# Kernel optimization log

Measured on AMD Instinct MI355X. Metric: run time of the kernel, lower is better.

## Reference

```python
import jax, jax.numpy as jnp
import numpy as np

N_ATOMS = 131072
N_EDGES = 524288
N_MOLS = 2048
D = 128      # n_atom_basis
F = 128      # n_filters
G = 50       # n_gaussians
T = 3        # interaction blocks
CUTOFF = 5.0
LOG2 = float(np.log(2.0))


def ssp(x):
    # shifted softplus: ln(0.5*e^x + 0.5) = softplus(x) - ln 2
    return jax.nn.softplus(x) - LOG2


def setup_inputs() -> dict:
    key = jax.random.key(0)
    ks = jax.random.split(key, 20)
    s = 0.05
    z = jax.random.randint(ks[0], (N_ATOMS,), 1, 100, dtype=jnp.int32)
    xyz = jax.random.normal(ks[1], (N_ATOMS, 3), dtype=jnp.float32) * 3.0
    a0 = jax.random.randint(ks[2], (N_EDGES,), 0, N_ATOMS, dtype=jnp.int32)
    off = jax.random.randint(ks[3], (N_EDGES,), 1, N_ATOMS, dtype=jnp.int32)
    a = jnp.stack([a0, (a0 + off) % N_ATOMS], axis=1)  # distinct endpoints
    mol_id = jnp.sort(jax.random.randint(ks[4], (N_ATOMS,), 0, N_MOLS, dtype=jnp.int32))
    emb = (jax.random.normal(ks[5], (100, D)) * s).at[0].set(0.0)  # padding_idx=0
    return dict(
        xyz=xyz,
        emb=emb,
        fw1=jax.random.normal(ks[6], (T, G, F)) * s,
        fb1=jnp.zeros((T, F)),
        fw2=jax.random.normal(ks[7], (T, F, F)) * s,
        fb2=jnp.zeros((T, F)),
        win=jax.random.normal(ks[8], (T, D, F)) * s,
        wout1=jax.random.normal(ks[9], (T, F, D)) * s,
        bout1=jnp.zeros((T, D)),
        wout2=jax.random.normal(ks[10], (T, D, D)) * s,
        bout2=jnp.zeros((T, D)),
        wa1=jax.random.normal(ks[11], (D, D // 2)) * s,
        ba1=jnp.zeros((D // 2,)),
        wa2=jax.random.normal(ks[12], (D // 2, 1)) * s,
        ba2=jnp.zeros((1,)),
        z=z, a=a, mol_id=mol_id,
    )


def reference(xyz, emb, fw1, fb1, fw2, fb2, win, wout1, bout1, wout2, bout2,
              wa1, ba1, wa2, ba2, z, a, mol_id):
    r = emb[z]                                            # [N, D] atom embeddings
    # edge distances: e = ||xyz[a0] - xyz[a1]||  -> [E, 1]
    d = jnp.sqrt(((xyz[a[:, 0]] - xyz[a[:, 1]]) ** 2).sum(-1))[:, None]
    # Gaussian smearing on [0, cutoff]
    offsets = jnp.linspace(0.0, CUTOFF, G)
    width = offsets[1] - offsets[0]
    g = jnp.exp((-0.5 / width ** 2) * (d - offsets) ** 2)  # [E, G]
    # smooth cosine cutoff (cutoff_soft)
    C = 0.5 * (jnp.cos(d * jnp.pi / CUTOFF) + 1.0)          # [E, 1]
    for t in range(T):
        # continuous filter network on edge features
        W = ssp(g @ fw1[t] + fb1[t]) @ fw2[t] + fb2[t]      # [E, F]
        W = W * C
        h = r @ win[t]                                      # in2f, no bias [N, F]
        # symmetric gather-filter-scatter over undirected edge list
        y = jnp.zeros_like(h)
        y = y.at[a[:, 0]].add(h[a[:, 1]] * W)
        y = y.at[a[:, 1]].add(h[a[:, 0]] * W)
        dr = ssp(y @ wout1[t] + bout1[t]) @ wout2[t] + bout2[t]
        r = r + dr                                          # residual update
    # atomwise energy head
    r = ssp(r @ wa1 + ba1) @ wa2 + ba2                      # [N, 1]
    # per-molecule sum pooling (torch.split + sum)
    return jax.ops.segment_sum(r, mol_id, num_segments=N_MOLS)  # [N_MOLS, 1]
```

## Files before the change

kernel.cpp:

```cpp
#include <hip/hip_runtime.h>
#include <hip/hip_bf16.h>

#define N_ATOMS 131072
#define N_EDGES 524288
#define N_MOLS  2048
#define DD      128
#define FF      128
#define GG      50
#define TT      3

typedef __hip_bfloat16 bf16;
typedef __attribute__((ext_vector_type(8))) short short8;
typedef __attribute__((ext_vector_type(4))) float floatx4;

__device__ __forceinline__ float b2f(bf16 v) { return __bfloat162float(v); }
__device__ __forceinline__ bf16  f2b(float v) { return __float2bfloat16(v); }

__device__ __forceinline__ unsigned short f2bu(float f) {
    unsigned u = __float_as_uint(f);
    u += 0x7fff + ((u >> 16) & 1);
    return (unsigned short)(u >> 16);
}
__device__ __forceinline__ bf16 f2b_fast(float f) {
    union { unsigned short u; bf16 b; } c; c.u = f2bu(f); return c.b;
}
__device__ __forceinline__ unsigned int pk2(float lo, float hi) {
    return ((unsigned)f2bu(hi) << 16) | f2bu(lo);
}

__device__ __forceinline__ float2 up2(unsigned int u) {
    float2 f;
    f.x = __uint_as_float(u << 16);
    f.y = __uint_as_float(u & 0xffff0000u);
    return f;
}

__device__ __forceinline__ float sspf(float x) {
    float e = __expf(-fabsf(x));
    return fmaxf(x, 0.f) + __logf(1.f + e) - 0.69314718056f;
}

__device__ __forceinline__ void fma8(float* ac, uint4 wv, uint4 hv) {
    float2 w0 = up2(wv.x), h0 = up2(hv.x);
    float2 w1 = up2(wv.y), h1 = up2(hv.y);
    float2 w2 = up2(wv.z), h2 = up2(hv.z);
    float2 w3 = up2(wv.w), h3 = up2(hv.w);
    ac[0] = fmaf(w0.x, h0.x, ac[0]); ac[1] = fmaf(w0.y, h0.y, ac[1]);
    ac[2] = fmaf(w1.x, h1.x, ac[2]); ac[3] = fmaf(w1.y, h1.y, ac[3]);
    ac[4] = fmaf(w2.x, h2.x, ac[4]); ac[5] = fmaf(w2.y, h2.y, ac[5]);
    ac[6] = fmaf(w3.x, h3.x, ac[6]); ac[7] = fmaf(w3.y, h3.y, ac[7]);
}

template <int NCT>
__device__ __forceinline__ void mfma_half(const bf16* A, const bf16* B,
                                          floatx4 (&acc)[2][NCT],
                                          int kA, int wave, int q, int ln) {
#pragma unroll
    for (int k0 = 0; k0 < 64; k0 += 32) {
        short8 a0 = *(const short8*)(A + (wave * 32 + ln) * 136 + kA + k0 + q * 8);
        short8 a1 = *(const short8*)(A + (wave * 32 + 16 + ln) * 136 + kA + k0 + q * 8);
#pragma unroll
        for (int ct = 0; ct < NCT; ct++) {
            short8 b = *(const short8*)(B + (ct * 16 + ln) * 72 + k0 + q * 8);
            acc[0][ct] = __builtin_amdgcn_mfma_f32_16x16x32_bf16(a0, b, acc[0][ct], 0, 0, 0);
            acc[1][ct] = __builtin_amdgcn_mfma_f32_16x16x32_bf16(a1, b, acc[1][ct], 0, 0, 0);
        }
    }
}

template <int NCT>
__device__ __forceinline__ void mfma_halfo(const bf16* A, const bf16* B,
                                           floatx4 (&acc)[2][8], int ctBase,
                                           int kA, int wave, int q, int ln) {
#pragma unroll
    for (int k0 = 0; k0 < 64; k0 += 32) {
        short8 a0 = *(const short8*)(A + (wave * 32 + ln) * 136 + kA + k0 + q * 8);
        short8 a1 = *(const short8*)(A + (wave * 32 + 16 + ln) * 136 + kA + k0 + q * 8);
#pragma unroll
        for (int ct = 0; ct < NCT; ct++) {
            short8 b = *(const short8*)(B + (ct * 16 + ln) * 72 + k0 + q * 8);
            acc[0][ctBase + ct] = __builtin_amdgcn_mfma_f32_16x16x32_bf16(a0, b, acc[0][ctBase + ct], 0, 0, 0);
            acc[1][ctBase + ct] = __builtin_amdgcn_mfma_f32_16x16x32_bf16(a1, b, acc[1][ctBase + ct], 0, 0, 0);
        }
    }
}

template <int NCT>
__device__ __forceinline__ void mfma64(const bf16* A, const bf16* B,
                                       floatx4 (&acc)[NCT],
                                       int kA, int wave, int q, int ln) {
#pragma unroll
    for (int k0 = 0; k0 < 64; k0 += 32) {
        short8 a = *(const short8*)(A + (wave * 16 + ln) * 136 + kA + k0 + q * 8);
#pragma unroll
        for (int ct = 0; ct < NCT; ct++) {
            short8 b = *(const short8*)(B + (ct * 16 + ln) * 72 + k0 + q * 8);
            acc[ct] = __builtin_amdgcn_mfma_f32_16x16x32_bf16(a, b, acc[ct], 0, 0, 0);
        }
    }
}

__device__ __forceinline__ void stage_b(bf16* B, const bf16* WT, int k0,
                                        int nrows, int ldk, int tid) {
    for (int i = tid; i < nrows * 8; i += 256) {
        int n = i >> 3, kc = i & 7;
        *(short8*)(B + n * 72 + kc * 8) =
            *(const short8*)(WT + n * ldk + k0 + kc * 8);
    }
}

__global__ __launch_bounds__(256) void k_initwt(const float* __restrict__ emb,
                                                const int* __restrict__ z,
                                                bf16* __restrict__ rb,
                                                const float* __restrict__ fw1,
                                                const float* __restrict__ fw2,
                                                const float* __restrict__ win,
                                                const float* __restrict__ wout1,
                                                const float* __restrict__ wout2,
                                                const float* __restrict__ wa1,
                                                bf16* __restrict__ fw1T, bf16* __restrict__ fw2T,
                                                bf16* __restrict__ winT, bf16* __restrict__ wout1T,
                                                bf16* __restrict__ wout2T, bf16* __restrict__ wa1T) {
    int bi = blockIdx.x;
    if (bi < N_ATOMS * 16 / 256) {
        int idx = bi * 256 + threadIdx.x;
        int atom = idx >> 4, seg = idx & 15;
        const float* src = emb + (size_t)z[atom] * DD + seg * 8;
        float4 v0 = *(const float4*)(src);
        float4 v1 = *(const float4*)(src + 4);
        uint4 o;
        o.x = pk2(v0.x, v0.y); o.y = pk2(v0.z, v0.w);
        o.z = pk2(v1.x, v1.y); o.w = pk2(v1.z, v1.w);
        *(uint4*)(rb + (size_t)atom * DD + seg * 8) = o;
        return;
    }
    int idx = (bi - N_ATOMS * 16 / 256) * 256 + threadIdx.x;
    if (idx < 3 * 128 * 64) {
        int t = idx / 8192, j = idx % 8192;
        int n = j >> 6, k = j & 63;
        fw1T[idx] = (k < GG) ? f2b(fw1[t * GG * FF + k * FF + n]) : f2b(0.f);
        return;
    }
    idx -= 3 * 128 * 64;
    if (idx < 3 * 16384) { int t = idx / 16384, j = idx % 16384; int n = j >> 7, k = j & 127;
        fw2T[idx] = f2b(fw2[t * 16384 + k * 128 + n]); return; }
    idx -= 3 * 16384;
    if (idx < 3 * 16384) { int t = idx / 16384, j = idx % 16384; int n = j >> 7, k = j & 127;
        winT[idx] = f2b(win[t * 16384 + k * 128 + n]); return; }
    idx -= 3 * 16384;
    if (idx < 3 * 16384) { int t = idx / 16384, j = idx % 16384; int n = j >> 7, k = j & 127;
        wout1T[idx] = f2b(wout1[t * 16384 + k * 128 + n]); return; }
    idx -= 3 * 16384;
    if (idx < 3 * 16384) { int t = idx / 16384, j = idx % 16384; int n = j >> 7, k = j & 127;
        wout2T[idx] = f2b(wout2[t * 16384 + k * 128 + n]); return; }
    idx -= 3 * 16384;
    if (idx < 64 * 128) { int n = idx >> 7, k = idx & 127;
        wa1T[idx] = f2b(wa1[k * 64 + n]); return; }
}

__global__ __launch_bounds__(256) void k_dist(const float* __restrict__ xyz,
                                              const int* __restrict__ a,
                                              float* __restrict__ dArr,
                                              float* __restrict__ cArr,
                                              float* __restrict__ molE) {
    int e = blockIdx.x * 256 + threadIdx.x;
    if (e < N_MOLS) molE[e] = 0.f;
    int A0 = a[2 * e], A1 = a[2 * e + 1];
    float dx = xyz[3 * A0]     - xyz[3 * A1];
    float dy = xyz[3 * A0 + 1] - xyz[3 * A1 + 1];
    float dz = xyz[3 * A0 + 2] - xyz[3 * A1 + 2];
    float d = sqrtf(dx * dx + dy * dy + dz * dz);
    dArr[e] = d;
    cArr[e] = 0.5f * (__cosf(d * 0.6283185307179586f) + 1.f);
}

__global__ __launch_bounds__(256) void k_zero2(int* __restrict__ pA,
                                               int* __restrict__ p1) {
    int i = blockIdx.x * 256 + threadIdx.x;
    if (i < N_ATOMS) pA[i] = 0;
    else p1[i - N_ATOMS] = 0;
}

__global__ __launch_bounds__(256) void k_count2(const int* __restrict__ a,
                                                int* __restrict__ cntA,
                                                int* __restrict__ cnt1,
                                                float* __restrict__ molE) {
    int e = blockIdx.x * 256 + threadIdx.x;
    if (e < N_MOLS) molE[e] = 0.f;
    atomicAdd(&cntA[a[2 * e]], 1);
    atomicAdd(&cnt1[a[2 * e + 1]], 1);
}

__global__ __launch_bounds__(256) void k_scan1j(const int* __restrict__ cursorA,
                                                const int* __restrict__ cursor1,
                                                int* __restrict__ bsumA,
                                                int* __restrict__ bsum1) {
    __shared__ int red[256];
    int tid = threadIdx.x;
    int arr = blockIdx.x >> 8, b = blockIdx.x & 255;
    const int* counts = arr ? cursor1 : cursorA;
    int* bsum = arr ? bsum1 : bsumA;
    int i0 = b * 512 + tid * 2;
    red[tid] = counts[i0] + counts[i0 + 1];
    __syncthreads();
    for (int off = 128; off > 0; off >>= 1) {
        if (tid < off) red[tid] += red[tid + off];
        __syncthreads();
    }
    if (tid == 0) bsum[b] = red[0];
}

__global__ __launch_bounds__(256) void k_scan2j(int* __restrict__ bsumA,
                                                int* __restrict__ bsum1,
                                                int* __restrict__ baseA,
                                                int* __restrict__ ptr1) {
    __shared__ int v[256];
    int tid = threadIdx.x;
    for (int arr = 0; arr < 2; arr++) {
        int* bsum = arr ? bsum1 : bsumA;
        int* ptrN = arr ? ptr1 : baseA;
        v[tid] = bsum[tid];
        __syncthreads();
        if (tid == 0) {
            int acc = 0;
            for (int i = 0; i < 256; i++) { int t = v[i]; v[i] = acc; acc += t; }
            ptrN[N_ATOMS] = acc;
        }
        __syncthreads();
        bsum[tid] = v[tid];
        __syncthreads();
    }
}

__global__ __launch_bounds__(256) void k_scan3j(int* __restrict__ cursorA,
                                                int* __restrict__ cursor1,
                                                const int* __restrict__ bsumA,
                                                const int* __restrict__ bsum1,
                                                int* __restrict__ baseA,
                                                int* __restrict__ ptr1) {
    __shared__ int red[256];
    int tid = threadIdx.x;
    int arr = blockIdx.x >> 8, b = blockIdx.x & 255;
    int* counts = arr ? cursor1 : cursorA;
    const int* bsum = arr ? bsum1 : bsumA;
    int* ptr = arr ? ptr1 : baseA;
    int i0 = b * 512 + tid * 2;
    int c0 = counts[i0], c1 = counts[i0 + 1];
    int s = c0 + c1;
    red[tid] = s;
    __syncthreads();
    for (int off = 1; off < 256; off <<= 1) {
        int t = (tid >= off) ? red[tid - off] : 0;
        __syncthreads();
        red[tid] += t;
        __syncthreads();
    }
    int base = bsum[b] + red[tid] - s;
    ptr[i0] = base;
    ptr[i0 + 1] = base + c0;
    counts[i0] = base;
    counts[i0 + 1] = base + c0;
}

__global__ __launch_bounds__(256) void k_permA(const float* __restrict__ xyz,
                                               const int* __restrict__ a,
                                               int* __restrict__ cursorA,
                                               int* __restrict__ cursor1,
                                               float* __restrict__ dAp,
                                               float* __restrict__ cAp,
                                               int* __restrict__ a1s,
                                               int* __restrict__ adj1) {
    int e = blockIdx.x * 256 + threadIdx.x;
    int A0 = a[2 * e], A1 = a[2 * e + 1];
    float dx = xyz[3 * A0]     - xyz[3 * A1];
    float dy = xyz[3 * A0 + 1] - xyz[3 * A1 + 1];
    float dz = xyz[3 * A0 + 2] - xyz[3 * A1 + 2];
    float d = sqrtf(dx * dx + dy * dy + dz * dz);
    int newe = atomicAdd(&cursorA[A0], 1);
    dAp[newe] = d;
    cAp[newe] = 0.5f * (__cosf(d * 0.6283185307179586f) + 1.f);
    a1s[newe] = A1;
    int slot = atomicAdd(&cursor1[A1], 1);
    adj1[2 * slot] = newe;
    adj1[2 * slot + 1] = A0;
}

struct SmemHE {
    bf16 A[128][136];
    bf16 B[64][72];
    float dS[128], cS[128], b1S[128], b2S[128];
};

__device__ __forceinline__ void h_part128(SmemHE& sm, int blk,
                                          const bf16* __restrict__ rb,
                                          const bf16* __restrict__ winT_t,
                                          bf16* __restrict__ h) {
    int tid = threadIdx.x, n0 = blk * 128;
    for (int i = tid; i < 128 * 16; i += 256) {
        int row = i >> 4, seg = i & 15;
        *(uint4*)(&sm.A[row][seg * 8]) =
            *(const uint4*)(rb + (size_t)(n0 + row) * DD + seg * 8);
    }
    stage_b(&sm.B[0][0], winT_t, 0, 64, 128, tid);
    __syncthreads();
    int wave = tid >> 6, lane = tid & 63, q = lane >> 4, ln = lane & 15;
    floatx4 acc[2][8];
#pragma unroll
    for (int i = 0; i < 2; i++)
#pragma unroll
        for (int j = 0; j < 8; j++) acc[i][j] = (floatx4){0.f, 0.f, 0.f, 0.f};
    mfma_halfo<4>(&sm.A[0][0], &sm.B[0][0], acc, 0, 0, wave, q, ln);
    __syncthreads();
    stage_b(&sm.B[0][0], winT_t + 64 * 128, 0, 64, 128, tid);
    __syncthreads();
    mfma_halfo<4>(&sm.A[0][0], &sm.B[0][0], acc, 4, 0, wave, q, ln);
    __syncthreads();
    stage_b(&sm.B[0][0], winT_t, 64, 64, 128, tid);
    __syncthreads();
    mfma_halfo<4>(&sm.A[0][0], &sm.B[0][0], acc, 0, 64, wave, q, ln);
    __syncthreads();
    stage_b(&sm.B[0][0], winT_t + 64 * 128, 64, 64, 128, tid);
    __syncthreads();
    mfma_halfo<4>(&sm.A[0][0], &sm.B[0][0], acc, 4, 64, wave, q, ln);
#pragma unroll
    for (int rt = 0; rt < 2; rt++)
#pragma unroll
        for (int cc = 0; cc < 8; cc++)
#pragma unroll
            for (int rg = 0; rg < 4; rg++) {
                int row = wave * 32 + rt * 16 + q * 4 + rg;
                int col = (cc >> 2) * 64 + (cc & 3) * 16 + ln;
                sm.A[row][col] = f2b_fast(acc[rt][cc][rg]);
            }
    __syncthreads();
    for (int i = tid; i < 128 * 16; i += 256) {
        int row = i >> 4, seg = i & 15;
        *(uint4*)(h + (size_t)(n0 + row) * FF + seg * 8) =
            *(const uint4*)(&sm.A[row][seg * 8]);
    }
}

__device__ __forceinline__ void edge_part128(SmemHE& sm, int blk,
                                             const float* __restrict__ dAp,
                                             const float* __restrict__ cAp,
                                             const bf16* __restrict__ fw1T_t,
                                             const float* __restrict__ fb1_t,
                                             const bf16* __restrict__ fw2T_t,
                                             const float* __restrict__ fb2_t,
                                             bf16* __restrict__ Wt) {
    int tid = threadIdx.x, e0 = blk * 128;
    if (tid < 128) {
        sm.dS[tid] = dAp[e0 + tid];
        sm.cS[tid] = cAp[e0 + tid];
        sm.b1S[tid] = fb1_t[tid];
        sm.b2S[tid] = fb2_t[tid];
    }
    stage_b(&sm.B[0][0], fw1T_t, 0, 64, 64, tid);
    __syncthreads();
    const float width = 5.0f / 49.0f;
    const float coeff = -0.5f / (width * width);
    for (int idx = tid; idx < 128 * 32; idx += 256) {
        int i = idx >> 5, kp = (idx & 31) * 2;
        float d = sm.dS[i];
        float t0 = d - (float)kp * width;
        float t1 = d - (float)(kp + 1) * width;
        float v0 = (kp < GG)     ? __expf(coeff * t0 * t0) : 0.f;
        float v1 = (kp + 1 < GG) ? __expf(coeff * t1 * t1) : 0.f;
        *(unsigned int*)(&sm.A[i][kp]) = pk2(v0, v1);
    }
    __syncthreads();
    int wave = tid >> 6, lane = tid & 63, q = lane >> 4, ln = lane & 15;
    floatx4 acc[2][8];
#pragma unroll
    for (int i = 0; i < 2; i++)
#pragma unroll
        for (int j = 0; j < 8; j++) acc[i][j] = (floatx4){0.f, 0.f, 0.f, 0.f};
    mfma_halfo<4>(&sm.A[0][0], &sm.B[0][0], acc, 0, 0, wave, q, ln);
    __syncthreads();
    stage_b(&sm.B[0][0], fw1T_t + 64 * 64, 0, 64, 64, tid);
    __syncthreads();
    mfma_halfo<4>(&sm.A[0][0], &sm.B[0][0], acc, 4, 0, wave, q, ln);
#pragma unroll
    for (int rt = 0; rt < 2; rt++)
#pragma unroll
        for (int cc = 0; cc < 8; cc++)
#pragma unroll
            for (int rg = 0; rg < 4; rg++) {
                int row = wave * 32 + rt * 16 + q * 4 + rg;
                int col = (cc >> 2) * 64 + (cc & 3) * 16 + ln;
                sm.A[row][col] = f2b_fast(sspf(acc[rt][cc][rg] + sm.b1S[col]));
            }
    __syncthreads();
    stage_b(&sm.B[0][0], fw2T_t, 0, 64, 128, tid);
    __syncthreads();
#pragma unroll
    for (int i = 0; i < 2; i++)
#pragma unroll
        for (int j = 0; j < 8; j++) acc[i][j] = (floatx4){0.f, 0.f, 0.f, 0.f};
    mfma_halfo<4>(&sm.A[0][0], &sm.B[0][0], acc, 0, 0, wave, q, ln);
    __syncthreads();
    stage_b(&sm.B[0][0], fw2T_t + 64 * 128, 0, 64, 128, tid);
    __syncthreads();
    mfma_halfo<4>(&sm.A[0][0], &sm.B[0][0], acc, 4, 0, wave, q, ln);
    __syncthreads();
    stage_b(&sm.B[0][0], fw2T_t, 64, 64, 128, tid);
    __syncthreads();
    mfma_halfo<4>(&sm.A[0][0], &sm.B[0][0], acc, 0, 64, wave, q, ln);
    __syncthreads();
    stage_b(&sm.B[0][0], fw2T_t + 64 * 128, 64, 64, 128, tid);
    __syncthreads();
    mfma_halfo<4>(&sm.A[0][0], &sm.B[0][0], acc, 4, 64, wave, q, ln);
#pragma unroll
    for (int rt = 0; rt < 2; rt++)
#pragma unroll
        for (int cc = 0; cc < 8; cc++)
#pragma unroll
            for (int rg = 0; rg < 4; rg++) {
                int row = wave * 32 + rt * 16 + q * 4 + rg;
                int col = (cc >> 2) * 64 + (cc & 3) * 16 + ln;
                sm.A[row][col] = f2b_fast((acc[rt][cc][rg] + sm.b2S[col]) * sm.cS[row]);
            }
    __syncthreads();
    for (int i = tid; i < 128 * 16; i += 256) {
        int row = i >> 4, seg = i & 15;
        *(uint4*)(Wt + (size_t)(e0 + row) * FF + seg * 8) =
            *(const uint4*)(&sm.A[row][seg * 8]);
    }
}

__global__ __launch_bounds__(256, 3) void k_he(const bf16* __restrict__ rb,
                                               const bf16* __restrict__ winT_t,
                                               bf16* __restrict__ h,
                                               const float* __restrict__ dAp,
                                               const float* __restrict__ cAp,
                                               const bf16* __restrict__ fw1T_t,
                                               const float* __restrict__ fb1_t,
                                               const bf16* __restrict__ fw2T_t,
                                               const float* __restrict__ fb2_t,
                                               bf16* __restrict__ Wt) {
    __shared__ SmemHE sm;
    int bi = blockIdx.x;
    if (bi % 5 == 0)
        h_part128(sm, bi / 5, rb, winT_t, h);
    else
        edge_part128(sm, bi - bi / 5 - 1, dAp, cAp, fw1T_t, fb1_t, fw2T_t, fb2_t, Wt);
}

__global__ __launch_bounds__(256, 5) void k_gather_node64(const int* __restrict__ baseA,
                                                          const int* __restrict__ a1s,
                                                          const int* __restrict__ ptr1,
                                                          const int* __restrict__ adj1,
                                                          const bf16* __restrict__ Wt,
                                                          const bf16* __restrict__ h,
                                                          const bf16* __restrict__ wout1T_t,
                                                          const float* __restrict__ bo1_t,
                                                          const bf16* __restrict__ wout2T_t,
                                                          const float* __restrict__ bo2_t,
                                                          bf16* __restrict__ rb) {
    __shared__ __align__(16) bf16 A[64][136];
    __shared__ __align__(16) bf16 B[64][72];
    __shared__ float b1S[128], b2S[128];
    int tid = threadIdx.x, n0 = blockIdx.x * 64;
    if (tid < 128) { b1S[tid] = bo1_t[tid]; b2S[tid] = bo2_t[tid]; }
    stage_b(&B[0][0], wout1T_t, 0, 64, 128, tid);
    int wave = tid >> 6, lane = tid & 63;
    int seg = lane & 15;
    int rg  = lane >> 4;
    for (int k = 0; k < 16; k += 2) {
        int rowA = wave * 16 + k;
        int atomA = n0 + rowA;
        int2 b01 = *(const int2*)(baseA + atomA);
        int b2v = baseA[atomA + 2];
        int2 p01 = *(const int2*)(ptr1 + atomA);
        int p2v = ptr1[atomA + 2];
        int sA0 = b01.x + rg, eA0v = b01.y;
        int sB0 = b01.y + rg, eB0v = b2v;
        int sA1 = p01.x + rg, eA1v = p01.y;
        int sB1 = p01.y + rg, eB1v = p2v;
        int oA = (sA0 < eA0v) ? a1s[sA0] : 0;
        int oB = (sB0 < eB0v) ? a1s[sB0] : 0;
        int2 eoA = (sA1 < eA1v) ? *(const int2*)(adj1 + 2 * sA1) : make_int2(0, 0);
        int2 eoB = (sB1 < eB1v) ? *(const int2*)(adj1 + 2 * sB1) : make_int2(0, 0);
        float acA[8], acB[8];
#pragma unroll
        for (int j = 0; j < 8; j++) { acA[j] = 0.f; acB[j] = 0.f; }
        while ((sA0 < eA0v) | (sA1 < eA1v) | (sB0 < eB0v) | (sB1 < eB1v)) {
            bool pA0 = sA0 < eA0v, pA1 = sA1 < eA1v;
            bool pB0 = sB0 < eB0v, pB1 = sB1 < eB1v;
            uint4 wvA0, hvA0, wvA1, hvA1, wvB0, hvB0, wvB1, hvB1;
            if (pA0) {
                wvA0 = *(const uint4*)(Wt + (size_t)sA0 * FF + seg * 8);
                hvA0 = *(const uint4*)(h + (size_t)oA * FF + seg * 8);
            }
            if (pA1) {
                wvA1 = *(const uint4*)(Wt + (size_t)eoA.x * FF + seg * 8);
                hvA1 = *(const uint4*)(h + (size_t)eoA.y * FF + seg * 8);
            }
            if (pB0) {
                wvB0 = *(const uint4*)(Wt + (size_t)sB0 * FF + seg * 8);
                hvB0 = *(const uint4*)(h + (size_t)oB * FF + seg * 8);
            }
            if (pB1) {
                wvB1 = *(const uint4*)(Wt + (size_t)eoB.x * FF + seg * 8);
                hvB1 = *(const uint4*)(h + (size_t)eoB.y * FF + seg * 8);
            }
            int sA0n = sA0 + 4, sA1n = sA1 + 4, sB0n = sB0 + 4, sB1n = sB1 + 4;
            int oAn = (sA0n < eA0v) ? a1s[sA0n] : 0;
            int oBn = (sB0n < eB0v) ? a1s[sB0n] : 0;
            int2 eoAn = (sA1n < eA1v) ? *(const int2*)(adj1 + 2 * sA1n) : make_int2(0, 0);
            int2 eoBn = (sB1n < eB1v) ? *(const int2*)(adj1 + 2 * sB1n) : make_int2(0, 0);
            if (pA0) fma8(acA, wvA0, hvA0);
            if (pA1) fma8(acA, wvA1, hvA1);
            if (pB0) fma8(acB, wvB0, hvB0);
            if (pB1) fma8(acB, wvB1, hvB1);
            sA0 = sA0n; sA1 = sA1n; sB0 = sB0n; sB1 = sB1n;
            oA = oAn; oB = oBn; eoA = eoAn; eoB = eoBn;
        }
#pragma unroll
        for (int j = 0; j < 8; j++) {
            float vA = acA[j], vB = acB[j];
            vA += __shfl_down(vA, 32); vB += __shfl_down(vB, 32);
            vA += __shfl_down(vA, 16); vB += __shfl_down(vB, 16);
            acA[j] = vA; acB[j] = vB;
        }
        if (rg == 0) {
            uint4 oU;
            oU.x = pk2(acA[0], acA[1]); oU.y = pk2(acA[2], acA[3]);
            oU.z = pk2(acA[4], acA[5]); oU.w = pk2(acA[6], acA[7]);
            *(uint4*)(&A[rowA][seg * 8]) = oU;
            oU.x = pk2(acB[0], acB[1]); oU.y = pk2(acB[2], acB[3]);
            oU.z = pk2(acB[4], acB[5]); oU.w = pk2(acB[6], acB[7]);
            *(uint4*)(&A[rowA + 1][seg * 8]) = oU;
        }
    }
    __syncthreads();
    int q = lane >> 4, ln = lane & 15;
    floatx4 acc[8];
#pragma unroll
    for (int j = 0; j < 8; j++) acc[j] = (floatx4){0.f, 0.f, 0.f, 0.f};
    mfma64<4>(&A[0][0], &B[0][0], *(floatx4(*)[4])(&acc[0]), 0, wave, q, ln);
    __syncthreads();
    stage_b(&B[0][0], wout1T_t + 64 * 128, 0, 64, 128, tid);
    __syncthreads();
    mfma64<4>(&A[0][0], &B[0][0], *(floatx4(*)[4])(&acc[4]), 0, wave, q, ln);
    __syncthreads();
    stage_b(&B[0][0], wout1T_t, 64, 64, 128, tid);
    __syncthreads();
    mfma64<4>(&A[0][0], &B[0][0], *(floatx4(*)[4])(&acc[0]), 64, wave, q, ln);
    __syncthreads();
    stage_b(&B[0][0], wout1T_t + 64 * 128, 64, 64, 128, tid);
    __syncthreads();
    mfma64<4>(&A[0][0], &B[0][0], *(floatx4(*)[4])(&acc[4]), 64, wave, q, ln);
#pragma unroll
    for (int cc = 0; cc < 8; cc++)
#pragma unroll
        for (int rgi = 0; rgi < 4; rgi++) {
            int row = wave * 16 + q * 4 + rgi;
            int col = (cc >> 2) * 64 + (cc & 3) * 16 + ln;
            A[row][col] = f2b_fast(sspf(acc[cc][rgi] + b1S[col]));
        }
    __syncthreads();
    stage_b(&B[0][0], wout2T_t, 0, 64, 128, tid);
    __syncthreads();
#pragma unroll
    for (int j = 0; j < 8; j++) acc[j] = (floatx4){0.f, 0.f, 0.f, 0.f};
    mfma64<4>(&A[0][0], &B[0][0], *(floatx4(*)[4])(&acc[0]), 0, wave, q, ln);
    __syncthreads();
    stage_b(&B[0][0], wout2T_t + 64 * 128, 0, 64, 128, tid);
    __syncthreads();
    mfma64<4>(&A[0][0], &B[0][0], *(floatx4(*)[4])(&acc[4]), 0, wave, q, ln);
    __syncthreads();
    stage_b(&B[0][0], wout2T_t, 64, 64, 128, tid);
    __syncthreads();
    mfma64<4>(&A[0][0], &B[0][0], *(floatx4(*)[4])(&acc[0]), 64, wave, q, ln);
    __syncthreads();
    stage_b(&B[0][0], wout2T_t + 64 * 128, 64, 64, 128, tid);
    __syncthreads();
    mfma64<4>(&A[0][0], &B[0][0], *(floatx4(*)[4])(&acc[4]), 64, wave, q, ln);
#pragma unroll
    for (int cc = 0; cc < 8; cc++)
#pragma unroll
        for (int rgi = 0; rgi < 4; rgi++) {
            int row = wave * 16 + q * 4 + rgi;
            int col = (cc >> 2) * 64 + (cc & 3) * 16 + ln;
            size_t off = (size_t)(n0 + row) * DD + col;
            rb[off] = f2b_fast(b2f(rb[off]) + acc[cc][rgi] + b2S[col]);
        }
}

__global__ __launch_bounds__(256) void k_h(const bf16* __restrict__ rb,
                                           const bf16* __restrict__ winT_t,
                                           bf16* __restrict__ h,
                                           float* __restrict__ y) {
    __shared__ __align__(16) bf16 A[128][136];
    __shared__ __align__(16) bf16 B[128][72];
    int tid = threadIdx.x, n0 = blockIdx.x * 128;
    for (int i = tid; i < 128 * 16; i += 256) {
        int row = i >> 4, seg = i & 15;
        *(uint4*)(&A[row][seg * 8]) =
            *(const uint4*)(rb + (size_t)(n0 + row) * DD + seg * 8);
        *(float4*)(y + (size_t)(n0 + row) * FF + seg * 8) = (float4){0.f, 0.f, 0.f, 0.f};
        *(float4*)(y + (size_t)(n0 + row) * FF + seg * 8 + 4) = (float4){0.f, 0.f, 0.f, 0.f};
    }
    stage_b(&B[0][0], winT_t, 0, 128, 128, tid);
    __syncthreads();
    int wave = tid >> 6, lane = tid & 63, q = lane >> 4, ln = lane & 15;
    floatx4 acc[2][8];
#pragma unroll
    for (int i = 0; i < 2; i++)
#pragma unroll
        for (int j = 0; j < 8; j++) acc[i][j] = (floatx4){0.f, 0.f, 0.f, 0.f};
    mfma_half<8>(&A[0][0], &B[0][0], acc, 0, wave, q, ln);
    __syncthreads();
    stage_b(&B[0][0], winT_t, 64, 128, 128, tid);
    __syncthreads();
    mfma_half<8>(&A[0][0], &B[0][0], acc, 64, wave, q, ln);
#pragma unroll
    for (int rt = 0; rt < 2; rt++)
#pragma unroll
        for (int ct = 0; ct < 8; ct++)
#pragma unroll
            for (int rg = 0; rg < 4; rg++) {
                int row = wave * 32 + rt * 16 + q * 4 + rg, col = ct * 16 + ln;
                h[(size_t)(n0 + row) * FF + col] = f2b(acc[rt][ct][rg]);
            }
}

__global__ __launch_bounds__(256) void k_edge(const float* __restrict__ dArr,
                                              const float* __restrict__ cArr,
                                              const int* __restrict__ a,
                                              const bf16* __restrict__ fw1T_t,
                                              const float* __restrict__ fb1_t,
                                              const bf16* __restrict__ fw2T_t,
                                              const float* __restrict__ fb2_t,
                                              const bf16* __restrict__ h,
                                              float* __restrict__ y) {
    __shared__ __align__(16) bf16 A[128][136];
    __shared__ __align__(16) bf16 B[128][72];
    __shared__ float dS[128], cS[128], b1S[128], b2S[128];
    __shared__ int a0S[128], a1S[128];
    int tid = threadIdx.x, e0 = blockIdx.x * 128;
    if (tid < 128) {
        int e = e0 + tid;
        dS[tid] = dArr[e]; cS[tid] = cArr[e];
        a0S[tid] = a[2 * e]; a1S[tid] = a[2 * e + 1];
        b1S[tid] = fb1_t[tid]; b2S[tid] = fb2_t[tid];
    }
    stage_b(&B[0][0], fw1T_t, 0, 128, 64, tid);
    __syncthreads();
    const float width = 5.0f / 49.0f;
    const float coeff = -0.5f / (width * width);
    for (int idx = tid; idx < 128 * 64; idx += 256) {
        int i = idx >> 6, k = idx & 63;
        float v = 0.f;
        if (k < GG) { float t = dS[i] - (float)k * width; v = __expf(coeff * t * t); }
        A[i][k] = f2b(v);
    }
    __syncthreads();
    int wave = tid >> 6, lane = tid & 63, q = lane >> 4, ln = lane & 15;
    floatx4 acc[2][8];
#pragma unroll
    for (int i = 0; i < 2; i++)
#pragma unroll
        for (int j = 0; j < 8; j++) acc[i][j] = (floatx4){0.f, 0.f, 0.f, 0.f};
    mfma_half<8>(&A[0][0], &B[0][0], acc, 0, wave, q, ln);
#pragma unroll
    for (int rt = 0; rt < 2; rt++)
#pragma unroll
        for (int ct = 0; ct < 8; ct++)
#pragma unroll
            for (int rg = 0; rg < 4; rg++) {
                int row = wave * 32 + rt * 16 + q * 4 + rg, col = ct * 16 + ln;
                A[row][col] = f2b(sspf(acc[rt][ct][rg] + b1S[col]));
            }
    __syncthreads();
    stage_b(&B[0][0], fw2T_t, 0, 128, 128, tid);
    __syncthreads();
#pragma unroll
    for (int i = 0; i < 2; i++)
#pragma unroll
        for (int j = 0; j < 8; j++) acc[i][j] = (floatx4){0.f, 0.f, 0.f, 0.f};
    mfma_half<8>(&A[0][0], &B[0][0], acc, 0, wave, q, ln);
    __syncthreads();
    stage_b(&B[0][0], fw2T_t, 64, 128, 128, tid);
    __syncthreads();
    mfma_half<8>(&A[0][0], &B[0][0], acc, 64, wave, q, ln);
#pragma unroll
    for (int rt = 0; rt < 2; rt++)
#pragma unroll
        for (int ct = 0; ct < 8; ct++)
#pragma unroll
            for (int rg = 0; rg < 4; rg++) {
                int row = wave * 32 + rt * 16 + q * 4 + rg, col = ct * 16 + ln;
                float w = (acc[rt][ct][rg] + b2S[col]) * cS[row];
                int A0 = a0S[row], A1 = a1S[row];
                float h0 = b2f(h[A0 * FF + col]);
                float h1 = b2f(h[A1 * FF + col]);
                atomicAdd(&y[A0 * FF + col], h1 * w);
                atomicAdd(&y[A1 * FF + col], h0 * w);
            }
}

__global__ __launch_bounds__(256) void k_node(const float* __restrict__ y,
                                              const bf16* __restrict__ wout1T_t,
                                              const float* __restrict__ bo1_t,
                                              const bf16* __restrict__ wout2T_t,
                                              const float* __restrict__ bo2_t,
                                              bf16* __restrict__ rb) {
    __shared__ __align__(16) bf16 A[128][136];
    __shared__ __align__(16) bf16 B[128][72];
    __shared__ float b1S[128], b2S[128];
    int tid = threadIdx.x, n0 = blockIdx.x * 128;
    if (tid < 128) { b1S[tid] = bo1_t[tid]; b2S[tid] = bo2_t[tid]; }
    for (int idx = tid; idx < 128 * 128; idx += 256) {
        int row = idx >> 7, col = idx & 127;
        A[row][col] = f2b(y[(size_t)(n0 + row) * FF + col]);
    }
    stage_b(&B[0][0], wout1T_t, 0, 128, 128, tid);
    __syncthreads();
    int wave = tid >> 6, lane = tid & 63, q = lane >> 4, ln = lane & 15;
    floatx4 acc[2][8];
#pragma unroll
    for (int i = 0; i < 2; i++)
#pragma unroll
        for (int j = 0; j < 8; j++) acc[i][j] = (floatx4){0.f, 0.f, 0.f, 0.f};
    mfma_half<8>(&A[0][0], &B[0][0], acc, 0, wave, q, ln);
    __syncthreads();
    stage_b(&B[0][0], wout1T_t, 64, 128, 128, tid);
    __syncthreads();
    mfma_half<8>(&A[0][0], &B[0][0], acc, 64, wave, q, ln);
#pragma unroll
    for (int rt = 0; rt < 2; rt++)
#pragma unroll
        for (int ct = 0; ct < 8; ct++)
#pragma unroll
            for (int rg = 0; rg < 4; rg++) {
                int row = wave * 32 + rt * 16 + q * 4 + rg, col = ct * 16 + ln;
                A[row][col] = f2b(sspf(acc[rt][ct][rg] + b1S[col]));
            }
    __syncthreads();
    stage_b(&B[0][0], wout2T_t, 0, 128, 128, tid);
    __syncthreads();
#pragma unroll
    for (int i = 0; i < 2; i++)
#pragma unroll
        for (int j = 0; j < 8; j++) acc[i][j] = (floatx4){0.f, 0.f, 0.f, 0.f};
    mfma_half<8>(&A[0][0], &B[0][0], acc, 0, wave, q, ln);
    __syncthreads();
    stage_b(&B[0][0], wout2T_t, 64, 128, 128, tid);
    __syncthreads();
    mfma_half<8>(&A[0][0], &B[0][0], acc, 64, wave, q, ln);
#pragma unroll
    for (int rt = 0; rt < 2; rt++)
#pragma unroll
        for (int ct = 0; ct < 8; ct++)
#pragma unroll
            for (int rg = 0; rg < 4; rg++) {
                int row = wave * 32 + rt * 16 + q * 4 + rg, col = ct * 16 + ln;
                size_t off = (size_t)(n0 + row) * DD + col;
                rb[off] = f2b_fast(b2f(rb[off]) + acc[rt][ct][rg] + b2S[col]);
            }
}

__global__ __launch_bounds__(256) void k_head(const bf16* __restrict__ rb,
                                              const bf16* __restrict__ wa1T,
                                              const float* __restrict__ ba1,
                                              const float* __restrict__ wa2,
                                              const float* __restrict__ ba2,
                                              const int* __restrict__ mol,
                                              float* __restrict__ molE) {
    __shared__ __align__(16) bf16 A[128][136];
    __shared__ __align__(16) bf16 B[64][72];
    __shared__ __align__(16) bf16 U[128][72];
    __shared__ float wa2S[64], ba1S[64];
    int tid = threadIdx.x, n0 = blockIdx.x * 128;
    if (tid < 64) { wa2S[tid] = wa2[tid]; ba1S[tid] = ba1[tid]; }
    for (int i = tid; i < 128 * 16; i += 256) {
        int row = i >> 4, seg = i & 15;
        *(uint4*)(&A[row][seg * 8]) =
            *(const uint4*)(rb + (size_t)(n0 + row) * DD + seg * 8);
    }
    stage_b(&B[0][0], wa1T, 0, 64, 128, tid);
    __syncthreads();
    int wave = tid >> 6, lane = tid & 63, q = lane >> 4, ln = lane & 15;
    floatx4 acc[2][4];
#pragma unroll
    for (int i = 0; i < 2; i++)
#pragma unroll
        for (int j = 0; j < 4; j++) acc[i][j] = (floatx4){0.f, 0.f, 0.f, 0.f};
    mfma_half<4>(&A[0][0], &B[0][0], acc, 0, wave, q, ln);
    __syncthreads();
    stage_b(&B[0][0], wa1T, 64, 64, 128, tid);
    __syncthreads();
    mfma_half<4>(&A[0][0], &B[0][0], acc, 64, wave, q, ln);
#pragma unroll
    for (int rt = 0; rt < 2; rt++)
#pragma unroll
        for (int ct = 0; ct < 4; ct++)
#pragma unroll
            for (int rg = 0; rg < 4; rg++) {
                int row = wave * 32 + rt * 16 + q * 4 + rg, col = ct * 16 + ln;
                U[row][col] = f2b_fast(acc[rt][ct][rg] + ba1S[col]);
            }
    __syncthreads();
    if (tid < 128) {
        float s = ba2[0];
#pragma unroll
        for (int j = 0; j < 64; j++) s += sspf(b2f(U[tid][j])) * wa2S[j];
        atomicAdd(&molE[mol[n0 + tid]], s);
    }
}

__global__ __launch_bounds__(256) void k_out(const float* __restrict__ molE,
                                             float* __restrict__ out) {
    int i = blockIdx.x * 256 + threadIdx.x;
    out[i] = molE[i];
}

extern "C" void kernel_launch(void* const* d_in, const int* in_sizes, int n_in,
                              void* d_out, int out_size, void* d_ws, size_t ws_size,
                              hipStream_t stream) {
    const float* xyz   = (const float*)d_in[0];
    const float* emb   = (const float*)d_in[1];
    const float* fw1   = (const float*)d_in[2];
    const float* fb1   = (const float*)d_in[3];
    const float* fw2   = (const float*)d_in[4];
    const float* fb2   = (const float*)d_in[5];
    const float* win   = (const float*)d_in[6];
    const float* wout1 = (const float*)d_in[7];
    const float* bout1 = (const float*)d_in[8];
    const float* wout2 = (const float*)d_in[9];
    const float* bout2 = (const float*)d_in[10];
    const float* wa1   = (const float*)d_in[11];
    const float* ba1   = (const float*)d_in[12];
    const float* wa2   = (const float*)d_in[13];
    const float* ba2   = (const float*)d_in[14];
    const int*  z     = (const int*)d_in[15];
    const int*  a     = (const int*)d_in[16];
    const int*  mol   = (const int*)d_in[17];

    char* ws = (char*)d_ws;
    bf16*  rb   = (bf16*) ws; ws += (size_t)N_ATOMS * DD * 2;
    bf16*  h    = (bf16*) ws; ws += (size_t)N_ATOMS * FF * 2;
    float* molE = (float*)ws; ws += (size_t)N_MOLS * 4;
    float* dAp  = (float*)ws; ws += (size_t)N_EDGES * 4;
    float* cAp  = (float*)ws; ws += (size_t)N_EDGES * 4;
    bf16*  fw1T   = (bf16*)ws; ws += 3 * 128 * 64 * 2;
    bf16*  fw2T   = (bf16*)ws; ws += 3 * 128 * 128 * 2;
    bf16*  winT   = (bf16*)ws; ws += 3 * 128 * 128 * 2;
    bf16*  wout1T = (bf16*)ws; ws += 3 * 128 * 128 * 2;
    bf16*  wout2T = (bf16*)ws; ws += 3 * 128 * 128 * 2;
    bf16*  wa1T   = (bf16*)ws; ws += 64 * 128 * 2;
    char*  csr_base = ws;
    int*   baseA   = (int*)ws; ws += 524320;
    int*   ptr1    = (int*)ws; ws += 524320;
    int*   cursorA = (int*)ws; ws += (size_t)N_ATOMS * 4;
    int*   cursor1 = (int*)ws; ws += (size_t)N_ATOMS * 4;
    int*   a1s     = (int*)ws; ws += (size_t)N_EDGES * 4;
    int*   adj1    = (int*)ws; ws += (size_t)2 * N_EDGES * 4;
    int*   bsumA   = (int*)ws; ws += 1024;
    int*   bsum1   = (int*)ws; ws += 1024;
    bf16*  Wt      = (bf16*)ws; ws += (size_t)N_EDGES * FF * 2;
    size_t need = (size_t)(ws - (char*)d_ws);

    k_initwt<<<N_ATOMS * 16 / 256 + 896, 256, 0, stream>>>(
        emb, z, rb, fw1, fw2, win, wout1, wout2, wa1,
        fw1T, fw2T, winT, wout1T, wout2T, wa1T);

    if (ws_size >= need) {
        k_zero2<<<2 * N_ATOMS / 256, 256, 0, stream>>>(cursorA, cursor1);
        k_count2<<<N_EDGES / 256, 256, 0, stream>>>(a, cursorA, cursor1, molE);
        k_scan1j<<<512, 256, 0, stream>>>(cursorA, cursor1, bsumA, bsum1);
        k_scan2j<<<1, 256, 0, stream>>>(bsumA, bsum1, baseA, ptr1);
        k_scan3j<<<512, 256, 0, stream>>>(cursorA, cursor1, bsumA, bsum1, baseA, ptr1);
        k_permA<<<N_EDGES / 256, 256, 0, stream>>>(xyz, a, cursorA, cursor1,
                                                   dAp, cAp, a1s, adj1);
        for (int t = 0; t < TT; t++) {
            k_he<<<N_ATOMS / 128 + N_EDGES / 128, 256, 0, stream>>>(
                rb, winT + t * 16384, h, dAp, cAp,
                fw1T + t * 8192, fb1 + t * FF,
                fw2T + t * 16384, fb2 + t * FF, Wt);
            k_gather_node64<<<N_ATOMS / 64, 256, 0, stream>>>(
                baseA, a1s, ptr1, adj1, Wt, h,
                wout1T + t * 16384, bout1 + t * DD,
                wout2T + t * 16384, bout2 + t * DD, rb);
        }
    } else {
        float* y = (float*)csr_base;
        k_dist<<<N_EDGES / 256, 256, 0, stream>>>(xyz, a, dAp, cAp, molE);
        for (int t = 0; t < TT; t++) {
            k_h<<<N_ATOMS / 128, 256, 0, stream>>>(rb, winT + t * 16384, h, y);
            k_edge<<<N_EDGES / 128, 256, 0, stream>>>(dAp, cAp, a,
                                                      fw1T + t * 8192, fb1 + t * FF,
                                                      fw2T + t * 16384, fb2 + t * FF, h, y);
            k_node<<<N_ATOMS / 128, 256, 0, stream>>>(y, wout1T + t * 16384, bout1 + t * DD,
                                                      wout2T + t * 16384, bout2 + t * DD, rb);
        }
    }
    k_head<<<N_ATOMS / 128, 256, 0, stream>>>(rb, wa1T, ba1, wa2, ba2, mol, molE);
    k_out<<<N_MOLS / 256, 256, 0, stream>>>(molE, (float*)d_out);
}
```

Measured before the change: 976.5 us.

## Use 512-thread blocks in fused h/edge kernel and drop output copy kernel

The fused h/edge-filter kernel now runs with 512 threads (8 waves), so each wave owns 16 rows of the 128-row tile instead of 32. Its accumulator registers are halved and more waves share the same LDS tile, which is meant to raise occupancy and latency hiding. In exchange, B-fragment reads from LDS are amortized over fewer rows per wave. The aggressive launch-bounds hint may also force register limits or spills. Separately, the molecule energies are accumulated directly into the output buffer, which removes the final copy kernel launch.

```diff
diff --git a/kernel.cpp b/kernel.cpp
--- a/kernel.cpp
+++ b/kernel.cpp
@@ -69,23 +69,6 @@
 }
 
 template <int NCT>
-__device__ __forceinline__ void mfma_halfo(const bf16* A, const bf16* B,
-                                           floatx4 (&acc)[2][8], int ctBase,
-                                           int kA, int wave, int q, int ln) {
-#pragma unroll
-    for (int k0 = 0; k0 < 64; k0 += 32) {
-        short8 a0 = *(const short8*)(A + (wave * 32 + ln) * 136 + kA + k0 + q * 8);
-        short8 a1 = *(const short8*)(A + (wave * 32 + 16 + ln) * 136 + kA + k0 + q * 8);
-#pragma unroll
-        for (int ct = 0; ct < NCT; ct++) {
-            short8 b = *(const short8*)(B + (ct * 16 + ln) * 72 + k0 + q * 8);
-            acc[0][ctBase + ct] = __builtin_amdgcn_mfma_f32_16x16x32_bf16(a0, b, acc[0][ctBase + ct], 0, 0, 0);
-            acc[1][ctBase + ct] = __builtin_amdgcn_mfma_f32_16x16x32_bf16(a1, b, acc[1][ctBase + ct], 0, 0, 0);
-        }
-    }
-}
-
-template <int NCT>
 __device__ __forceinline__ void mfma64(const bf16* A, const bf16* B,
                                        floatx4 (&acc)[NCT],
                                        int kA, int wave, int q, int ln) {
@@ -103,6 +86,15 @@
 __device__ __forceinline__ void stage_b(bf16* B, const bf16* WT, int k0,
                                         int nrows, int ldk, int tid) {
     for (int i = tid; i < nrows * 8; i += 256) {
+        int n = i >> 3, kc = i & 7;
+        *(short8*)(B + n * 72 + kc * 8) =
+            *(const short8*)(WT + n * ldk + k0 + kc * 8);
+    }
+}
+
+__device__ __forceinline__ void stage_b512(bf16* B, const bf16* WT, int k0,
+                                           int nrows, int ldk, int tid) {
+    for (int i = tid; i < nrows * 8; i += 512) {
         int n = i >> 3, kc = i & 7;
         *(short8*)(B + n * 72 + kc * 8) =
             *(const short8*)(WT + n * ldk + k0 + kc * 8);
@@ -291,56 +283,52 @@
     float dS[128], cS[128], b1S[128], b2S[128];
 };
 
-__device__ __forceinline__ void h_part128(SmemHE& sm, int blk,
+__device__ __forceinline__ void h_part512(SmemHE& sm, int blk,
                                           const bf16* __restrict__ rb,
                                           const bf16* __restrict__ winT_t,
                                           bf16* __restrict__ h) {
     int tid = threadIdx.x, n0 = blk * 128;
-    for (int i = tid; i < 128 * 16; i += 256) {
+    for (int i = tid; i < 128 * 16; i += 512) {
         int row = i >> 4, seg = i & 15;
         *(uint4*)(&sm.A[row][seg * 8]) =
             *(const uint4*)(rb + (size_t)(n0 + row) * DD + seg * 8);
     }
-    stage_b(&sm.B[0][0], winT_t, 0, 64, 128, tid);
+    stage_b512(&sm.B[0][0], winT_t, 0, 64, 128, tid);
     __syncthreads();
     int wave = tid >> 6, lane = tid & 63, q = lane >> 4, ln = lane & 15;
-    floatx4 acc[2][8];
-#pragma unroll
-    for (int i = 0; i < 2; i++)
-#pragma unroll
-        for (int j = 0; j < 8; j++) acc[i][j] = (floatx4){0.f, 0.f, 0.f, 0.f};
-    mfma_halfo<4>(&sm.A[0][0], &sm.B[0][0], acc, 0, 0, wave, q, ln);
-    __syncthreads();
-    stage_b(&sm.B[0][0], winT_t + 64 * 128, 0, 64, 128, tid);
-    __syncthreads();
-    mfma_halfo<4>(&sm.A[0][0], &sm.B[0][0], acc, 4, 0, wave, q, ln);
-    __syncthreads();
-    stage_b(&sm.B[0][0], winT_t, 64, 64, 128, tid);
-    __syncthreads();
-    mfma_halfo<4>(&sm.A[0][0], &sm.B[0][0], acc, 0, 64, wave, q, ln);
-    __syncthreads();
-    stage_b(&sm.B[0][0], winT_t + 64 * 128, 64, 64, 128, tid);
-    __syncthreads();
-    mfma_halfo<4>(&sm.A[0][0], &sm.B[0][0], acc, 4, 64, wave, q, ln);
-#pragma unroll
-    for (int rt = 0; rt < 2; rt++)
-#pragma unroll
-        for (int cc = 0; cc < 8; cc++)
-#pragma unroll
-            for (int rg = 0; rg < 4; rg++) {
-                int row = wave * 32 + rt * 16 + q * 4 + rg;
-                int col = (cc >> 2) * 64 + (cc & 3) * 16 + ln;
-                sm.A[row][col] = f2b_fast(acc[rt][cc][rg]);
-            }
-    __syncthreads();
-    for (int i = tid; i < 128 * 16; i += 256) {
+    floatx4 acc[8];
+#pragma unroll
+    for (int j = 0; j < 8; j++) acc[j] = (floatx4){0.f, 0.f, 0.f, 0.f};
+    mfma64<4>(&sm.A[0][0], &sm.B[0][0], *(floatx4(*)[4])(&acc[0]), 0, wave, q, ln);
+    __syncthreads();
+    stage_b512(&sm.B[0][0], winT_t + 64 * 128, 0, 64, 128, tid);
+    __syncthreads();
+    mfma64<4>(&sm.A[0][0], &sm.B[0][0], *(floatx4(*)[4])(&acc[4]), 0, wave, q, ln);
+    __syncthreads();
+    stage_b512(&sm.B[0][0], winT_t, 64, 64, 128, tid);
+    __syncthreads();
+    mfma64<4>(&sm.A[0][0], &sm.B[0][0], *(floatx4(*)[4])(&acc[0]), 64, wave, q, ln);
+    __syncthreads();
+    stage_b512(&sm.B[0][0], winT_t + 64 * 128, 64, 64, 128, tid);
+    __syncthreads();
+    mfma64<4>(&sm.A[0][0], &sm.B[0][0], *(floatx4(*)[4])(&acc[4]), 64, wave, q, ln);
+#pragma unroll
+    for (int cc = 0; cc < 8; cc++)
+#pragma unroll
+        for (int rg = 0; rg < 4; rg++) {
+            int row = wave * 16 + q * 4 + rg;
+            int col = (cc >> 2) * 64 + (cc & 3) * 16 + ln;
+            sm.A[row][col] = f2b_fast(acc[cc][rg]);
+        }
+    __syncthreads();
+    for (int i = tid; i < 128 * 16; i += 512) {
         int row = i >> 4, seg = i & 15;
         *(uint4*)(h + (size_t)(n0 + row) * FF + seg * 8) =
             *(const uint4*)(&sm.A[row][seg * 8]);
     }
 }
 
-__device__ __forceinline__ void edge_part128(SmemHE& sm, int blk,
+__device__ __forceinline__ void edge_part512(SmemHE& sm, int blk,
                                              const float* __restrict__ dAp,
                                              const float* __restrict__ cAp,
                                              const bf16* __restrict__ fw1T_t,
@@ -355,11 +343,11 @@
         sm.b1S[tid] = fb1_t[tid];
         sm.b2S[tid] = fb2_t[tid];
     }
-    stage_b(&sm.B[0][0], fw1T_t, 0, 64, 64, tid);
+    stage_b512(&sm.B[0][0], fw1T_t, 0, 64, 64, tid);
     __syncthreads();
     const float width = 5.0f / 49.0f;
     const float coeff = -0.5f / (width * width);
-    for (int idx = tid; idx < 128 * 32; idx += 256) {
+    for (int idx = tid; idx < 128 * 32; idx += 512) {
         int i = idx >> 5, kp = (idx & 31) * 2;
         float d = sm.dS[i];
         float t0 = d - (float)kp * width;
@@ -370,65 +358,57 @@
     }
     __syncthreads();
     int wave = tid >> 6, lane = tid & 63, q = lane >> 4, ln = lane & 15;
-    floatx4 acc[2][8];
-#pragma unroll
-    for (int i = 0; i < 2; i++)
-#pragma unroll
-        for (int j = 0; j < 8; j++) acc[i][j] = (floatx4){0.f, 0.f, 0.f, 0.f};
-    mfma_halfo<4>(&sm.A[0][0], &sm.B[0][0], acc, 0, 0, wave, q, ln);
-    __syncthreads();
-    stage_b(&sm.B[0][0], fw1T_t + 64 * 64, 0, 64, 64, tid);
-    __syncthreads();
-    mfma_halfo<4>(&sm.A[0][0], &sm.B[0][0], acc, 4, 0, wave, q, ln);
-#pragma unroll
-    for (int rt = 0; rt < 2; rt++)
-#pragma unroll
-        for (int cc = 0; cc < 8; cc++)
-#pragma unroll
-            for (int rg = 0; rg < 4; rg++) {
-                int row = wave * 32 + rt * 16 + q * 4 + rg;
-                int col = (cc >> 2) * 64 + (cc & 3) * 16 + ln;
-                sm.A[row][col] = f2b_fast(sspf(acc[rt][cc][rg] + sm.b1S[col]));
-            }
-    __syncthreads();
-    stage_b(&sm.B[0][0], fw2T_t, 0, 64, 128, tid);
-    __syncthreads();
-#pragma unroll
-    for (int i = 0; i < 2; i++)
-#pragma unroll
-        for (int j = 0; j < 8; j++) acc[i][j] = (floatx4){0.f, 0.f, 0.f, 0.f};
-    mfma_halfo<4>(&sm.A[0][0], &sm.B[0][0], acc, 0, 0, wave, q, ln);
-    __syncthreads();
-    stage_b(&sm.B[0][0], fw2T_t + 64 * 128, 0, 64, 128, tid);
-    __syncthreads();
-    mfma_halfo<4>(&sm.A[0][0], &sm.B[0][0], acc, 4, 0, wave, q, ln);
-    __syncthreads();
-    stage_b(&sm.B[0][0], fw2T_t, 64, 64, 128, tid);
-    __syncthreads();
-    mfma_halfo<4>(&sm.A[0][0], &sm.B[0][0], acc, 0, 64, wave, q, ln);
-    __syncthreads();
-    stage_b(&sm.B[0][0], fw2T_t + 64 * 128, 64, 64, 128, tid);
-    __syncthreads();
-    mfma_halfo<4>(&sm.A[0][0], &sm.B[0][0], acc, 4, 64, wave, q, ln);
-#pragma unroll
-    for (int rt = 0; rt < 2; rt++)
-#pragma unroll
-        for (int cc = 0; cc < 8; cc++)
-#pragma unroll
-            for (int rg = 0; rg < 4; rg++) {
-                int row = wave * 32 + rt * 16 + q * 4 + rg;
-                int col = (cc >> 2) * 64 + (cc & 3) * 16 + ln;
-                sm.A[row][col] = f2b_fast((acc[rt][cc][rg] + sm.b2S[col]) * sm.cS[row]);
-            }
-    __syncthreads();
-    for (int i = tid; i < 128 * 16; i += 256) {
+    floatx4 acc[8];
+#pragma unroll
+    for (int j = 0; j < 8; j++) acc[j] = (floatx4){0.f, 0.f, 0.f, 0.f};
+    mfma64<4>(&sm.A[0][0], &sm.B[0][0], *(floatx4(*)[4])(&acc[0]), 0, wave, q, ln);
+    __syncthreads();
+    stage_b512(&sm.B[0][0], fw1T_t + 64 * 64, 0, 64, 64, tid);
+    __syncthreads();
+    mfma64<4>(&sm.A[0][0], &sm.B[0][0], *(floatx4(*)[4])(&acc[4]), 0, wave, q, ln);
+#pragma unroll
+    for (int cc = 0; cc < 8; cc++)
+#pragma unroll
+        for (int rg = 0; rg < 4; rg++) {
+            int row = wave * 16 + q * 4 + rg;
+            int col = (cc >> 2) * 64 + (cc & 3) * 16 + ln;
+            sm.A[row][col] = f2b_fast(sspf(acc[cc][rg] + sm.b1S[col]));
+        }
+    __syncthreads();
+    stage_b512(&sm.B[0][0], fw2T_t, 0, 64, 128, tid);
+    __syncthreads();
+#pragma unroll
+    for (int j = 0; j < 8; j++) acc[j] = (floatx4){0.f, 0.f, 0.f, 0.f};
+    mfma64<4>(&sm.A[0][0], &sm.B[0][0], *(floatx4(*)[4])(&acc[0]), 0, wave, q, ln);
+    __syncthreads();
+    stage_b512(&sm.B[0][0], fw2T_t + 64 * 128, 0, 64, 128, tid);
+    __syncthreads();
+    mfma64<4>(&sm.A[0][0], &sm.B[0][0], *(floatx4(*)[4])(&acc[4]), 0, wave, q, ln);
+    __syncthreads();
+    stage_b512(&sm.B[0][0], fw2T_t, 64, 64, 128, tid);
+    __syncthreads();
+    mfma64<4>(&sm.A[0][0], &sm.B[0][0], *(floatx4(*)[4])(&acc[0]), 64, wave, q, ln);
+    __syncthreads();
+    stage_b512(&sm.B[0][0], fw2T_t + 64 * 128, 64, 64, 128, tid);
+    __syncthreads();
+    mfma64<4>(&sm.A[0][0], &sm.B[0][0], *(floatx4(*)[4])(&acc[4]), 64, wave, q, ln);
+#pragma unroll
+    for (int cc = 0; cc < 8; cc++)
+#pragma unroll
+        for (int rg = 0; rg < 4; rg++) {
+            int row = wave * 16 + q * 4 + rg;
+            int col = (cc >> 2) * 64 + (cc & 3) * 16 + ln;
+            sm.A[row][col] = f2b_fast((acc[cc][rg] + sm.b2S[col]) * sm.cS[row]);
+        }
+    __syncthreads();
+    for (int i = tid; i < 128 * 16; i += 512) {
         int row = i >> 4, seg = i & 15;
         *(uint4*)(Wt + (size_t)(e0 + row) * FF + seg * 8) =
             *(const uint4*)(&sm.A[row][seg * 8]);
     }
 }
 
-__global__ __launch_bounds__(256, 3) void k_he(const bf16* __restrict__ rb,
+__global__ __launch_bounds__(512, 6) void k_he(const bf16* __restrict__ rb,
                                                const bf16* __restrict__ winT_t,
                                                bf16* __restrict__ h,
                                                const float* __restrict__ dAp,
@@ -441,9 +421,9 @@
     __shared__ SmemHE sm;
     int bi = blockIdx.x;
     if (bi % 5 == 0)
-        h_part128(sm, bi / 5, rb, winT_t, h);
+        h_part512(sm, bi / 5, rb, winT_t, h);
     else
-        edge_part128(sm, bi - bi / 5 - 1, dAp, cAp, fw1T_t, fb1_t, fw2T_t, fb2_t, Wt);
+        edge_part512(sm, bi - bi / 5 - 1, dAp, cAp, fw1T_t, fb1_t, fw2T_t, fb2_t, Wt);
 }
 
 __global__ __launch_bounds__(256, 5) void k_gather_node64(const int* __restrict__ baseA,
@@ -811,12 +791,6 @@
     }
 }
 
-__global__ __launch_bounds__(256) void k_out(const float* __restrict__ molE,
-                                             float* __restrict__ out) {
-    int i = blockIdx.x * 256 + threadIdx.x;
-    out[i] = molE[i];
-}
-
 extern "C" void kernel_launch(void* const* d_in, const int* in_sizes, int n_in,
                               void* d_out, int out_size, void* d_ws, size_t ws_size,
                               hipStream_t stream) {
@@ -839,10 +813,11 @@
     const int*  a     = (const int*)d_in[16];
     const int*  mol   = (const int*)d_in[17];
 
+    float* molE = (float*)d_out;
+
     char* ws = (char*)d_ws;
     bf16*  rb   = (bf16*) ws; ws += (size_t)N_ATOMS * DD * 2;
     bf16*  h    = (bf16*) ws; ws += (size_t)N_ATOMS * FF * 2;
-    float* molE = (float*)ws; ws += (size_t)N_MOLS * 4;
     float* dAp  = (float*)ws; ws += (size_t)N_EDGES * 4;
     float* cAp  = (float*)ws; ws += (size_t)N_EDGES * 4;
     bf16*  fw1T   = (bf16*)ws; ws += 3 * 128 * 64 * 2;
@@ -876,7 +851,7 @@
         k_permA<<<N_EDGES / 256, 256, 0, stream>>>(xyz, a, cursorA, cursor1,
                                                    dAp, cAp, a1s, adj1);
         for (int t = 0; t < TT; t++) {
-            k_he<<<N_ATOMS / 128 + N_EDGES / 128, 256, 0, stream>>>(
+            k_he<<<N_ATOMS / 128 + N_EDGES / 128, 512, 0, stream>>>(
                 rb, winT + t * 16384, h, dAp, cAp,
                 fw1T + t * 8192, fb1 + t * FF,
                 fw2T + t * 16384, fb2 + t * FF, Wt);
@@ -898,5 +873,4 @@
         }
     }
     k_head<<<N_ATOMS / 128, 256, 0, stream>>>(rb, wa1T, ba1, wa2, ba2, mol, molE);
-    k_out<<<N_MOLS / 256, 256, 0, stream>>>(molE, (float*)d_out);
-}
+}
```

New measurement: 958.0 us, median of 2. No clear change (-1.9%).
